# Performance work log

Measured on AMD Instinct MI355X. Metric: run time of the kernel, lower is better.

Reference implementation:

```python
import jax, jax.numpy as jnp
import numpy as np

B, N, D_IN = 4, 512, 64
D_ATT, D_HID, D_ATT_NUM = 32, 128, 2
A_HID = 64
MASK_CONST = 10000.0


def _mlp2(x, W1, b1, W2, b2):
    # 2-layer MLP (Linear-ReLU-Linear), as built by cfg_Block('mlp', ...)
    return jax.nn.relu(x @ W1 + b1) @ W2 + b2


def setup_inputs() -> dict:
    key = jax.random.key(0)
    ks = jax.random.split(key, 32)
    s = 0.1

    def w(k, shp):
        return (jax.random.normal(k, shp, dtype=jnp.float32) * s)

    inp = {"x": jax.random.normal(ks[0], (B, N, D_IN), dtype=jnp.float32)}
    # key / query / value encoders: 64 -> 128 -> 32
    for i, p in enumerate(["k", "q", "v"]):
        inp[p + "W1"] = w(ks[1 + 2 * i], (D_IN, D_HID)); inp[p + "b1"] = jnp.zeros((D_HID,), jnp.float32)
        inp[p + "W2"] = w(ks[2 + 2 * i], (D_HID, D_ATT)); inp[p + "b2"] = jnp.zeros((D_ATT,), jnp.float32)
    # attention MLP: 2*D_att -> 64 -> D_att_num
    inp["aW1"] = w(ks[7], (2 * D_ATT, A_HID)); inp["ab1"] = jnp.zeros((A_HID,), jnp.float32)
    inp["aW2"] = w(ks[8], (A_HID, D_ATT_NUM)); inp["ab2"] = jnp.zeros((D_ATT_NUM,), jnp.float32)
    # decoders (x and y): 2*D_att -> 128 -> 64, then mu/sig heads 64 -> 1
    for i, p in enumerate(["dx", "dy"]):
        inp[p + "W1"] = w(ks[9 + 2 * i], (2 * D_ATT, D_HID)); inp[p + "b1"] = jnp.zeros((D_HID,), jnp.float32)
        inp[p + "W2"] = w(ks[10 + 2 * i], (D_HID, A_HID)); inp[p + "b2"] = jnp.zeros((A_HID,), jnp.float32)
    for i, p in enumerate(["mx", "sx", "my", "sy"]):
        inp[p + "W"] = w(ks[13 + i], (A_HID, 1)); inp[p + "b"] = jnp.zeros((1,), jnp.float32)
    return inp


def reference(x, kW1, kb1, kW2, kb2, qW1, qb1, qW2, qb2, vW1, vb1, vW2, vb2,
              aW1, ab1, aW2, ab2, dxW1, dxb1, dxW2, dxb2, dyW1, dyb1, dyW2, dyb2,
              mxW, mxb, sxW, sxb, myW, myb, syW, syb):
    k = _mlp2(x, kW1, kb1, kW2, kb2)  # [B,N,D_att]
    q = _mlp2(x, qW1, qb1, qW2, qb2)
    v = _mlp2(x, vW1, vb1, vW2, vb2)

    # z[b,i,j] = cat(k[b,i], q[b,j]); first att layer applied without
    # materializing z: z@aW1 = k@aW1[:D] + q@aW1[D:]
    hk = k @ aW1[:D_ATT]          # [B,N,A_HID]
    hq = q @ aW1[D_ATT:]          # [B,N,A_HID]
    h = jax.nn.relu(hk[:, :, None, :] + hq[:, None, :, :] + ab1)  # [B,N,N,A_HID]
    score = h @ aW2 + ab2          # [B,N,N,D_att_num]

    mask = jnp.eye(N, dtype=x.dtype)[None, :, :, None] * MASK_CONST
    w = jax.nn.sigmoid(score - mask)  # [B,N,N,D_att_num]

    agg0 = jnp.einsum('bij,bjd->bid', w[..., 0], v)
    agg1 = jnp.einsum('bij,bjd->bid', w[..., 1], v)
    c0 = jnp.concatenate([v, agg0], axis=-1)  # [B,N,2*D_att]
    c1 = jnp.concatenate([v, agg1], axis=-1)

    d_x = _mlp2(c0, dxW1, dxb1, dxW2, dxb2)
    mu_x = jnp.squeeze(d_x @ mxW + mxb, -1)                 # [B,N]
    sig_x = jnp.squeeze(jax.nn.softplus(d_x @ sxW + sxb), -1)
    d_y = _mlp2(c1, dyW1, dyb1, dyW2, dyb2)
    mu_y = jnp.squeeze(d_y @ myW + myb, -1)
    sig_y = jnp.squeeze(jax.nn.softplus(d_y @ syW + syb), -1)
    return ((mu_x, sig_x), (mu_y, sig_y))
```

## Files before the change

kernel.cpp:

```cpp
#include <hip/hip_runtime.h>
#include <hip/hip_bf16.h>

#define BB 4
#define NN 512

#define WS_V    0
#define WS_HK   65536
#define WS_HQ   196608
#define WS_AGG  327680

__global__ __launch_bounds__(128) void k_enc(
    const float* __restrict__ x,
    const float* __restrict__ kW1, const float* __restrict__ kb1,
    const float* __restrict__ kW2, const float* __restrict__ kb2,
    const float* __restrict__ qW1, const float* __restrict__ qb1,
    const float* __restrict__ qW2, const float* __restrict__ qb2,
    const float* __restrict__ vW1, const float* __restrict__ vb1,
    const float* __restrict__ vW2, const float* __restrict__ vb2,
    const float* __restrict__ aW1, const float* __restrict__ ab1,
    float* __restrict__ wsf)
{
  const int t = threadIdx.x;
  const int r0 = blockIdx.x * 4;
  __shared__ float xs[4][64];
  __shared__ float h1s[4][132];
  __shared__ float encs[3][4][32];

  if (t < 64) {
    float4 f = ((const float4*)x)[(size_t)r0 * 16 + t];
    int m = t * 4;
    xs[m >> 6][m & 63] = f.x; xs[(m + 1) >> 6][(m + 1) & 63] = f.y;
    xs[(m + 2) >> 6][(m + 2) & 63] = f.z; xs[(m + 3) >> 6][(m + 3) & 63] = f.w;
  }
  __syncthreads();

  #pragma unroll
  for (int e = 0; e < 3; ++e) {
    const float* W1 = (e == 0) ? kW1 : (e == 1) ? qW1 : vW1;
    const float* b1 = (e == 0) ? kb1 : (e == 1) ? qb1 : vb1;
    const float* W2 = (e == 0) ? kW2 : (e == 1) ? qW2 : vW2;
    const float* b2 = (e == 0) ? kb2 : (e == 1) ? qb2 : vb2;

    {
      float acc[4];
      float bb = b1[t];
      #pragma unroll
      for (int r = 0; r < 4; ++r) acc[r] = bb;
      #pragma unroll 4
      for (int i = 0; i < 64; ++i) {
        float wv = W1[i * 128 + t];
        #pragma unroll
        for (int r = 0; r < 4; ++r) acc[r] = fmaf(xs[r][i], wv, acc[r]);
      }
      #pragma unroll
      for (int r = 0; r < 4; ++r) h1s[r][t] = fmaxf(acc[r], 0.f);
    }
    __syncthreads();

    {
      const int c = t & 31, rr = t >> 5;
      float a0 = b2[c];
      #pragma unroll 4
      for (int i = 0; i < 128; ++i) {
        float wv = W2[i * 32 + c];
        a0 = fmaf(h1s[rr][i], wv, a0);
      }
      encs[e][rr][c] = a0;
    }
    __syncthreads();
  }

  {
    int r = t >> 5, cc = t & 31;
    wsf[WS_V + (r0 + r) * 32 + cc] = encs[2][r][cc];
  }

  {
    const int h = t & 63, half = t >> 6;
    const int eidx = half;
    float s4[4];
    float bias = half ? 0.f : ab1[h];
    #pragma unroll
    for (int kk = 0; kk < 4; ++kk) s4[kk] = bias;
    const float* aw = aW1 + (half ? 32 * 64 : 0);
    #pragma unroll 4
    for (int cc = 0; cc < 32; ++cc) {
      float wv = aw[cc * 64 + h];
      #pragma unroll
      for (int kk = 0; kk < 4; ++kk)
        s4[kk] = fmaf(encs[eidx][kk][cc], wv, s4[kk]);
    }
    float* dst = wsf + (half ? WS_HQ : WS_HK);
    #pragma unroll
    for (int kk = 0; kk < 4; ++kk)
      dst[(size_t)(r0 + kk) * 64 + h] = s4[kk];
  }
}

__global__ __launch_bounds__(256, 4) void k_att(
    const float* __restrict__ v_ws, const float* __restrict__ hk_ws,
    const float* __restrict__ hq_ws, const float* __restrict__ aW2,
    const float* __restrict__ ab2, float* __restrict__ aggh)
{
  const int t = threadIdx.x;
  const int bid = blockIdx.x;
  const int jq = bid & 3;
  const int it = (bid >> 2) & 127;
  const int b  = bid >> 9;
  const int i0 = it * 4;
  const int jbase = jq * 128;

  const int q   = t & 3;
  const int jj1 = (t >> 2) & 15;
  const int ii1 = t >> 6;
  const int ig  = i0 + ii1;

  const int dd  = t & 15;
  const int c2  = (t >> 4) & 1;
  const int jh  = (t >> 5) & 1;
  const int i2  = t >> 6;

  __shared__ float hqs[2][16][68];
  __shared__ float vs[2][16][36];
  __shared__ float ws_w[2][4][20];

  float hk16[16];
  {
    const float4* hkp = (const float4*)(hk_ws + ((size_t)b * NN + ig) * 64 + q * 16);
    #pragma unroll
    for (int m = 0; m < 4; ++m) {
      float4 f = hkp[m];
      hk16[4 * m] = f.x; hk16[4 * m + 1] = f.y;
      hk16[4 * m + 2] = f.z; hk16[4 * m + 3] = f.w;
    }
  }
  float aw0[16], aw1[16];
  {
    const float4* awp = (const float4*)(aW2 + q * 32);
    #pragma unroll
    for (int k = 0; k < 8; ++k) {
      float4 f = awp[k];
      aw0[2 * k] = f.x;     aw1[2 * k] = f.y;
      aw0[2 * k + 1] = f.z; aw1[2 * k + 1] = f.w;
    }
  }
  const float sb0 = ab2[0], sb1 = ab2[1];

  float accx = 0.f, accy = 0.f;
  const bool vload = (t < 128);

  {
    float4 hq_r = *(const float4*)(hq_ws + ((size_t)b * NN + jbase + (t >> 4)) * 64 + (t & 15) * 4);
    *(float4*)(&hqs[0][t >> 4][(t & 15) * 4]) = hq_r;
    if (vload) {
      float4 v_r = *(const float4*)(v_ws + ((size_t)b * NN + jbase + (t >> 3)) * 32 + (t & 7) * 4);
      *(float4*)(&vs[0][t >> 3][(t & 7) * 4]) = v_r;
    }
  }
  __syncthreads();

  int p = 0;
  for (int jt = 0; jt < 8; ++jt) {
    const int j0 = jbase + jt * 16;

    float4 hq_n, v_n;
    if (jt < 7) {
      const int j0n = j0 + 16;
      hq_n = *(const float4*)(hq_ws + ((size_t)b * NN + j0n + (t >> 4)) * 64 + (t & 15) * 4);
      if (vload)
        v_n = *(const float4*)(v_ws + ((size_t)b * NN + j0n + (t >> 3)) * 32 + (t & 7) * 4);
    }

    {
      float s0 = 0.f, s1 = 0.f;
      #pragma unroll
      for (int mc = 0; mc < 4; ++mc) {
        float4 hq4 = *(const float4*)(&hqs[p][jj1][q * 16 + mc * 4]);
        float z;
        z = fmaxf(hk16[4 * mc + 0] + hq4.x, 0.f);
        s0 = fmaf(z, aw0[4 * mc + 0], s0); s1 = fmaf(z, aw1[4 * mc + 0], s1);
        z = fmaxf(hk16[4 * mc + 1] + hq4.y, 0.f);
        s0 = fmaf(z, aw0[4 * mc + 1], s0); s1 = fmaf(z, aw1[4 * mc + 1], s1);
        z = fmaxf(hk16[4 * mc + 2] + hq4.z, 0.f);
        s0 = fmaf(z, aw0[4 * mc + 2], s0); s1 = fmaf(z, aw1[4 * mc + 2], s1);
        z = fmaxf(hk16[4 * mc + 3] + hq4.w, 0.f);
        s0 = fmaf(z, aw0[4 * mc + 3], s0); s1 = fmaf(z, aw1[4 * mc + 3], s1);
      }
      s0 += __shfl_xor(s0, 1); s0 += __shfl_xor(s0, 2);
      s1 += __shfl_xor(s1, 1); s1 += __shfl_xor(s1, 2);
      s0 += sb0; s1 += sb1;
      float sel = (q & 1) ? s1 : s0;
      float w = 1.f / (1.f + __expf(-sel));
      if (ig == j0 + jj1) w = 0.f;
      if (q < 2) ws_w[q][ii1][jj1] = w;
    }
    __syncthreads();

    {
      float4 w4a = *(const float4*)(&ws_w[c2][i2][jh * 8]);
      float4 w4b = *(const float4*)(&ws_w[c2][i2][jh * 8 + 4]);
      const int jb = jh * 8;
      float2 vv;
      vv = *(const float2*)(&vs[p][jb + 0][2 * dd]);
      accx = fmaf(w4a.x, vv.x, accx); accy = fmaf(w4a.x, vv.y, accy);
      vv = *(const float2*)(&vs[p][jb + 1][2 * dd]);
      accx = fmaf(w4a.y, vv.x, accx); accy = fmaf(w4a.y, vv.y, accy);
      vv = *(const float2*)(&vs[p][jb + 2][2 * dd]);
      accx = fmaf(w4a.z, vv.x, accx); accy = fmaf(w4a.z, vv.y, accy);
      vv = *(const float2*)(&vs[p][jb + 3][2 * dd]);
      accx = fmaf(w4a.w, vv.x, accx); accy = fmaf(w4a.w, vv.y, accy);
      vv = *(const float2*)(&vs[p][jb + 4][2 * dd]);
      accx = fmaf(w4b.x, vv.x, accx); accy = fmaf(w4b.x, vv.y, accy);
      vv = *(const float2*)(&vs[p][jb + 5][2 * dd]);
      accx = fmaf(w4b.y, vv.x, accx); accy = fmaf(w4b.y, vv.y, accy);
      vv = *(const float2*)(&vs[p][jb + 6][2 * dd]);
      accx = fmaf(w4b.z, vv.x, accx); accy = fmaf(w4b.z, vv.y, accy);
      vv = *(const float2*)(&vs[p][jb + 7][2 * dd]);
      accx = fmaf(w4b.w, vv.x, accx); accy = fmaf(w4b.w, vv.y, accy);
    }

    if (jt < 7) {
      *(float4*)(&hqs[p ^ 1][t >> 4][(t & 15) * 4]) = hq_n;
      if (vload) *(float4*)(&vs[p ^ 1][t >> 3][(t & 7) * 4]) = v_n;
    }
    __syncthreads();
    p ^= 1;
  }

  accx += __shfl_xor(accx, 32);
  accy += __shfl_xor(accy, 32);
  if (jh == 0) {
    const size_t row = (size_t)b * NN + i0 + i2;
    float2 o; o.x = accx; o.y = accy;
    *(float2*)(&aggh[((size_t)(c2 * 4 + jq) * 2048 + row) * 32 + 2 * dd]) = o;
  }
}

__global__ __launch_bounds__(256) void k_dec(
    const float* __restrict__ v_ws, const float* __restrict__ aggh,
    const float* __restrict__ dxW1, const float* __restrict__ dxb1,
    const float* __restrict__ dxW2, const float* __restrict__ dxb2,
    const float* __restrict__ dyW1, const float* __restrict__ dyb1,
    const float* __restrict__ dyW2, const float* __restrict__ dyb2,
    const float* __restrict__ mxW, const float* __restrict__ mxb,
    const float* __restrict__ sxW, const float* __restrict__ sxb,
    const float* __restrict__ myW, const float* __restrict__ myb,
    const float* __restrict__ syW, const float* __restrict__ syb,
    float* __restrict__ out)
{
  const int t = threadIdx.x;
  const int r0 = blockIdx.x * 4;
  const int half = t >> 7;
  const int u = t & 127;

  __shared__ float ccs[2][4][64];
  __shared__ float h1s[2][4][132];
  __shared__ float dds[2][4][64];

  {
    const float* aggp = aggh + (size_t)half * 4 * 65536;
    for (int m = u; m < 256; m += 128) {
      int r = m >> 6, i = m & 63;
      size_t row = (size_t)(r0 + r);
      float val;
      if (i < 32) {
        val = v_ws[row * 32 + i];
      } else {
        int o = i - 32;
        val = aggp[row * 32 + o] + aggp[65536 + row * 32 + o]
            + aggp[131072 + row * 32 + o] + aggp[196608 + row * 32 + o];
      }
      ccs[half][r][i] = val;
    }
  }
  __syncthreads();

  const float* W1 = half ? dyW1 : dxW1;
  const float* b1 = half ? dyb1 : dxb1;
  const float* W2 = half ? dyW2 : dxW2;
  const float* b2 = half ? dyb2 : dxb2;

  {
    float acc[4];
    float bb = b1[u];
    #pragma unroll
    for (int r = 0; r < 4; ++r) acc[r] = bb;
    #pragma unroll 4
    for (int i = 0; i < 64; ++i) {
      float wv = W1[i * 128 + u];
      #pragma unroll
      for (int r = 0; r < 4; ++r) acc[r] = fmaf(ccs[half][r][i], wv, acc[r]);
    }
    #pragma unroll
    for (int r = 0; r < 4; ++r) h1s[half][r][u] = fmaxf(acc[r], 0.f);
  }
  __syncthreads();

  {
    const int cI = u & 63, rr = u >> 6;
    float a0 = b2[cI], a1 = a0;
    #pragma unroll 4
    for (int i = 0; i < 128; ++i) {
      float wv = W2[i * 64 + cI];
      a0 = fmaf(h1s[half][rr * 2 + 0][i], wv, a0);
      a1 = fmaf(h1s[half][rr * 2 + 1][i], wv, a1);
    }
    dds[half][rr * 2 + 0][cI] = a0;
    dds[half][rr * 2 + 1][cI] = a1;
  }
  __syncthreads();

  {
    const int w = t >> 6, halfw = w >> 1, rr = w & 1, lane = t & 63;
    const float* mW = halfw ? myW : mxW;
    const float* sW = halfw ? syW : sxW;
    const float* mb = halfw ? myb : mxb;
    const float* sb = halfw ? syb : sxb;
    float mwv = mW[lane], swv = sW[lane];
    #pragma unroll
    for (int kk = 0; kk < 2; ++kk) {
      int r = rr * 2 + kk;
      float dval = dds[halfw][r][lane];
      float pm = dval * mwv, ps = dval * swv;
      #pragma unroll
      for (int msk = 32; msk >= 1; msk >>= 1) {
        pm += __shfl_xor(pm, msk);
        ps += __shfl_xor(ps, msk);
      }
      if (lane == 0) {
        float mu = pm + mb[0];
        float z = ps + sb[0];
        float sp = (z > 20.f) ? z : log1pf(__expf(z));
        out[halfw * 4096 + (r0 + r)] = mu;
        out[halfw * 4096 + 2048 + (r0 + r)] = sp;
      }
    }
  }
}

extern "C" void kernel_launch(void* const* d_in, const int* in_sizes, int n_in,
                              void* d_out, int out_size, void* d_ws, size_t ws_size,
                              hipStream_t stream) {
  (void)in_sizes; (void)n_in; (void)out_size; (void)ws_size;
  const float* x   = (const float*)d_in[0];
  const float* kW1 = (const float*)d_in[1];  const float* kb1 = (const float*)d_in[2];
  const float* kW2 = (const float*)d_in[3];  const float* kb2 = (const float*)d_in[4];
  const float* qW1 = (const float*)d_in[5];  const float* qb1 = (const float*)d_in[6];
  const float* qW2 = (const float*)d_in[7];  const float* qb2 = (const float*)d_in[8];
  const float* vW1 = (const float*)d_in[9];  const float* vb1 = (const float*)d_in[10];
  const float* vW2 = (const float*)d_in[11]; const float* vb2 = (const float*)d_in[12];
  const float* aW1 = (const float*)d_in[13]; const float* ab1 = (const float*)d_in[14];
  const float* aW2 = (const float*)d_in[15]; const float* ab2 = (const float*)d_in[16];
  const float* dxW1 = (const float*)d_in[17]; const float* dxb1 = (const float*)d_in[18];
  const float* dxW2 = (const float*)d_in[19]; const float* dxb2 = (const float*)d_in[20];
  const float* dyW1 = (const float*)d_in[21]; const float* dyb1 = (const float*)d_in[22];
  const float* dyW2 = (const float*)d_in[23]; const float* dyb2 = (const float*)d_in[24];
  const float* mxW = (const float*)d_in[25]; const float* mxb = (const float*)d_in[26];
  const float* sxW = (const float*)d_in[27]; const float* sxb = (const float*)d_in[28];
  const float* myW = (const float*)d_in[29]; const float* myb = (const float*)d_in[30];
  const float* syW = (const float*)d_in[31]; const float* syb = (const float*)d_in[32];

  float* wsf = (float*)d_ws;
  float* out = (float*)d_out;

  hipLaunchKernelGGL(k_enc, dim3(512), dim3(128), 0, stream,
                     x, kW1, kb1, kW2, kb2, qW1, qb1, qW2, qb2, vW1, vb1, vW2, vb2,
                     aW1, ab1, wsf);
  hipLaunchKernelGGL(k_att, dim3(2048), dim3(256), 0, stream,
                     wsf + WS_V, wsf + WS_HK, wsf + WS_HQ, aW2, ab2,
                     wsf + WS_AGG);
  hipLaunchKernelGGL(k_dec, dim3(512), dim3(256), 0, stream,
                     wsf + WS_V, wsf + WS_AGG,
                     dxW1, dxb1, dxW2, dxb2, dyW1, dyb1, dyW2, dyb2,
                     mxW, mxb, sxW, sxb, myW, myb, syW, syb, out);
}
```

Before: 203.2 us.

## Split encoder per MLP and decoder per head/row-pair for more blocks

```diff
diff --git a/kernel.cpp b/kernel.cpp
--- a/kernel.cpp
+++ b/kernel.cpp
@@ -9,7 +9,7 @@
 #define WS_HQ   196608
 #define WS_AGG  327680
 
-__global__ __launch_bounds__(128) void k_enc(
+__global__ __launch_bounds__(256) void k_enc(
     const float* __restrict__ x,
     const float* __restrict__ kW1, const float* __restrict__ kb1,
     const float* __restrict__ kW2, const float* __restrict__ kb2,
@@ -21,79 +21,69 @@
     float* __restrict__ wsf)
 {
   const int t = threadIdx.x;
-  const int r0 = blockIdx.x * 4;
-  __shared__ float xs[4][64];
-  __shared__ float h1s[4][132];
-  __shared__ float encs[3][4][32];
-
-  if (t < 64) {
-    float4 f = ((const float4*)x)[(size_t)r0 * 16 + t];
-    int m = t * 4;
-    xs[m >> 6][m & 63] = f.x; xs[(m + 1) >> 6][(m + 1) & 63] = f.y;
-    xs[(m + 2) >> 6][(m + 2) & 63] = f.z; xs[(m + 3) >> 6][(m + 3) & 63] = f.w;
-  }
-  __syncthreads();
-
-  #pragma unroll
-  for (int e = 0; e < 3; ++e) {
-    const float* W1 = (e == 0) ? kW1 : (e == 1) ? qW1 : vW1;
-    const float* b1 = (e == 0) ? kb1 : (e == 1) ? qb1 : vb1;
-    const float* W2 = (e == 0) ? kW2 : (e == 1) ? qW2 : vW2;
-    const float* b2 = (e == 0) ? kb2 : (e == 1) ? qb2 : vb2;
-
-    {
-      float acc[4];
-      float bb = b1[t];
+  const int bid = blockIdx.x;
+  const int e  = bid >> 8;
+  const int r0 = (bid & 255) * 8;
+
+  __shared__ float xs[8][64];
+  __shared__ float h1s[8][132];
+  __shared__ float encs[8][33];
+
+  const float* W1 = (e == 0) ? kW1 : (e == 1) ? qW1 : vW1;
+  const float* b1 = (e == 0) ? kb1 : (e == 1) ? qb1 : vb1;
+  const float* W2 = (e == 0) ? kW2 : (e == 1) ? qW2 : vW2;
+  const float* b2 = (e == 0) ? kb2 : (e == 1) ? qb2 : vb2;
+
+  {
+    float2 f = ((const float2*)x)[(size_t)r0 * 32 + t];
+    int m = t * 2;
+    xs[m >> 6][m & 63] = f.x;
+    xs[(m + 1) >> 6][(m + 1) & 63] = f.y;
+  }
+  __syncthreads();
+
+  {
+    const int h = t & 127, rh = t >> 7;
+    float acc[4];
+    float bb = b1[h];
+    #pragma unroll
+    for (int r = 0; r < 4; ++r) acc[r] = bb;
+    #pragma unroll 4
+    for (int i = 0; i < 64; ++i) {
+      float wv = W1[i * 128 + h];
       #pragma unroll
-      for (int r = 0; r < 4; ++r) acc[r] = bb;
-      #pragma unroll 4
-      for (int i = 0; i < 64; ++i) {
-        float wv = W1[i * 128 + t];
-        #pragma unroll
-        for (int r = 0; r < 4; ++r) acc[r] = fmaf(xs[r][i], wv, acc[r]);
-      }
-      #pragma unroll
-      for (int r = 0; r < 4; ++r) h1s[r][t] = fmaxf(acc[r], 0.f);
-    }
+      for (int r = 0; r < 4; ++r) acc[r] = fmaf(xs[rh * 4 + r][i], wv, acc[r]);
+    }
+    #pragma unroll
+    for (int r = 0; r < 4; ++r) h1s[rh * 4 + r][h] = fmaxf(acc[r], 0.f);
+  }
+  __syncthreads();
+
+  {
+    const int row = t >> 5, c = t & 31;
+    float a = b2[c];
+    #pragma unroll 4
+    for (int i = 0; i < 128; ++i)
+      a = fmaf(h1s[row][i], W2[i * 32 + c], a);
+    if (e == 2) wsf[WS_V + (size_t)(r0 + row) * 32 + c] = a;
+    else        encs[row][c] = a;
+  }
+
+  if (e != 2) {
     __syncthreads();
-
-    {
-      const int c = t & 31, rr = t >> 5;
-      float a0 = b2[c];
-      #pragma unroll 4
-      for (int i = 0; i < 128; ++i) {
-        float wv = W2[i * 32 + c];
-        a0 = fmaf(h1s[rr][i], wv, a0);
-      }
-      encs[e][rr][c] = a0;
-    }
-    __syncthreads();
-  }
-
-  {
-    int r = t >> 5, cc = t & 31;
-    wsf[WS_V + (r0 + r) * 32 + cc] = encs[2][r][cc];
-  }
-
-  {
-    const int h = t & 63, half = t >> 6;
-    const int eidx = half;
-    float s4[4];
-    float bias = half ? 0.f : ab1[h];
-    #pragma unroll
-    for (int kk = 0; kk < 4; ++kk) s4[kk] = bias;
-    const float* aw = aW1 + (half ? 32 * 64 : 0);
+    const int h = t & 63, rp = t >> 6;
+    float bias = (e == 0) ? ab1[h] : 0.f;
+    float s0 = bias, s1 = bias;
+    const float* aw = aW1 + (e ? 32 * 64 : 0);
     #pragma unroll 4
     for (int cc = 0; cc < 32; ++cc) {
       float wv = aw[cc * 64 + h];
-      #pragma unroll
-      for (int kk = 0; kk < 4; ++kk)
-        s4[kk] = fmaf(encs[eidx][kk][cc], wv, s4[kk]);
-    }
-    float* dst = wsf + (half ? WS_HQ : WS_HK);
-    #pragma unroll
-    for (int kk = 0; kk < 4; ++kk)
-      dst[(size_t)(r0 + kk) * 64 + h] = s4[kk];
+      s0 = fmaf(encs[rp * 2 + 0][cc], wv, s0);
+      s1 = fmaf(encs[rp * 2 + 1][cc], wv, s1);
+    }
+    float* dst = wsf + (e ? WS_HQ : WS_HK);
+    dst[(size_t)(r0 + rp * 2 + 0) * 64 + h] = s0;
+    dst[(size_t)(r0 + rp * 2 + 1) * 64 + h] = s1;
   }
 }
 
@@ -249,29 +239,27 @@
     float* __restrict__ out)
 {
   const int t = threadIdx.x;
-  const int r0 = blockIdx.x * 4;
-  const int half = t >> 7;
-  const int u = t & 127;
-
-  __shared__ float ccs[2][4][64];
-  __shared__ float h1s[2][4][132];
-  __shared__ float dds[2][4][64];
-
-  {
+  const int bid = blockIdx.x;
+  const int half = bid & 1;
+  const int r0 = (bid >> 1) * 2;
+
+  __shared__ float ccs[2][64];
+  __shared__ float h1s[2][132];
+  __shared__ float dds[2][64];
+
+  if (t < 128) {
     const float* aggp = aggh + (size_t)half * 4 * 65536;
-    for (int m = u; m < 256; m += 128) {
-      int r = m >> 6, i = m & 63;
-      size_t row = (size_t)(r0 + r);
-      float val;
-      if (i < 32) {
-        val = v_ws[row * 32 + i];
-      } else {
-        int o = i - 32;
-        val = aggp[row * 32 + o] + aggp[65536 + row * 32 + o]
-            + aggp[131072 + row * 32 + o] + aggp[196608 + row * 32 + o];
-      }
-      ccs[half][r][i] = val;
-    }
+    int r = t >> 6, i = t & 63;
+    size_t row = (size_t)(r0 + r);
+    float val;
+    if (i < 32) {
+      val = v_ws[row * 32 + i];
+    } else {
+      int o = i - 32;
+      val = aggp[row * 32 + o] + aggp[65536 + row * 32 + o]
+          + aggp[131072 + row * 32 + o] + aggp[196608 + row * 32 + o];
+    }
+    ccs[r][i] = val;
   }
   __syncthreads();
 
@@ -281,47 +269,34 @@
   const float* b2 = half ? dyb2 : dxb2;
 
   {
-    float acc[4];
-    float bb = b1[u];
-    #pragma unroll
-    for (int r = 0; r < 4; ++r) acc[r] = bb;
-    #pragma unroll 4
-    for (int i = 0; i < 64; ++i) {
-      float wv = W1[i * 128 + u];
-      #pragma unroll
-      for (int r = 0; r < 4; ++r) acc[r] = fmaf(ccs[half][r][i], wv, acc[r]);
-    }
-    #pragma unroll
-    for (int r = 0; r < 4; ++r) h1s[half][r][u] = fmaxf(acc[r], 0.f);
-  }
-  __syncthreads();
-
-  {
-    const int cI = u & 63, rr = u >> 6;
-    float a0 = b2[cI], a1 = a0;
-    #pragma unroll 4
-    for (int i = 0; i < 128; ++i) {
-      float wv = W2[i * 64 + cI];
-      a0 = fmaf(h1s[half][rr * 2 + 0][i], wv, a0);
-      a1 = fmaf(h1s[half][rr * 2 + 1][i], wv, a1);
-    }
-    dds[half][rr * 2 + 0][cI] = a0;
-    dds[half][rr * 2 + 1][cI] = a1;
-  }
-  __syncthreads();
-
-  {
-    const int w = t >> 6, halfw = w >> 1, rr = w & 1, lane = t & 63;
-    const float* mW = halfw ? myW : mxW;
-    const float* sW = halfw ? syW : sxW;
-    const float* mb = halfw ? myb : mxb;
-    const float* sb = halfw ? syb : sxb;
-    float mwv = mW[lane], swv = sW[lane];
-    #pragma unroll
-    for (int kk = 0; kk < 2; ++kk) {
-      int r = rr * 2 + kk;
-      float dval = dds[halfw][r][lane];
-      float pm = dval * mwv, ps = dval * swv;
+    const int h = t & 127, r = t >> 7;
+    float acc = b1[h];
+    #pragma unroll 4
+    for (int i = 0; i < 64; ++i)
+      acc = fmaf(ccs[r][i], W1[i * 128 + h], acc);
+    h1s[r][h] = fmaxf(acc, 0.f);
+  }
+  __syncthreads();
+
+  if (t < 128) {
+    const int r = t >> 6, c = t & 63;
+    float a = b2[c];
+    #pragma unroll 4
+    for (int i = 0; i < 128; ++i)
+      a = fmaf(h1s[r][i], W2[i * 64 + c], a);
+    dds[r][c] = a;
+  }
+  __syncthreads();
+
+  {
+    const int w = t >> 6, lane = t & 63;
+    if (w < 2) {
+      const float* mW = half ? myW : mxW;
+      const float* sW = half ? syW : sxW;
+      const float* mb = half ? myb : mxb;
+      const float* sb = half ? syb : sxb;
+      float dval = dds[w][lane];
+      float pm = dval * mW[lane], ps = dval * sW[lane];
       #pragma unroll
       for (int msk = 32; msk >= 1; msk >>= 1) {
         pm += __shfl_xor(pm, msk);
@@ -331,8 +306,8 @@
         float mu = pm + mb[0];
         float z = ps + sb[0];
         float sp = (z > 20.f) ? z : log1pf(__expf(z));
-        out[halfw * 4096 + (r0 + r)] = mu;
-        out[halfw * 4096 + 2048 + (r0 + r)] = sp;
+        out[half * 4096 + (r0 + w)] = mu;
+        out[half * 4096 + 2048 + (r0 + w)] = sp;
       }
     }
   }
@@ -363,13 +338,13 @@
   float* wsf = (float*)d_ws;
   float* out = (float*)d_out;
 
-  hipLaunchKernelGGL(k_enc, dim3(512), dim3(128), 0, stream,
+  hipLaunchKernelGGL(k_enc, dim3(768), dim3(256), 0, stream,
                      x, kW1, kb1, kW2, kb2, qW1, qb1, qW2, qb2, vW1, vb1, vW2, vb2,
                      aW1, ab1, wsf);
   hipLaunchKernelGGL(k_att, dim3(2048), dim3(256), 0, stream,
                      wsf + WS_V, wsf + WS_HK, wsf + WS_HQ, aW2, ab2,
                      wsf + WS_AGG);
-  hipLaunchKernelGGL(k_dec, dim3(512), dim3(256), 0, stream,
+  hipLaunchKernelGGL(k_dec, dim3(2048), dim3(256), 0, stream,
                      wsf + WS_V, wsf + WS_AGG,
                      dxW1, dxb1, dxW2, dxb2, dyW1, dyb1, dyW2, dyb2,
                      mxW, mxb, sxW, sxb, myW, myb, syW, syb, out);
```

Result: faster. 175.0 us (-13.9%).
